# Optimization experiments

Hardware: AMD Instinct MI355X
Metric: run time of the kernel (lower is better)

The kernel has to match this reference:

```python
import jax, jax.numpy as jnp
import numpy as np

INPUT_DIM, HID, LAT, FUT = 32, 128, 64, 128
B, T = 1024, 512


def _linear(x, W, b):
    return x @ W.T + b


def _lstm_layer(xs, Wih, Whh, b):
    # xs: [T, B, D_in] -> ys: [T, B, HID], h_T: [B, HID]
    Bsz = xs.shape[1]
    h0 = jnp.zeros((Bsz, HID), xs.dtype)
    c0 = jnp.zeros((Bsz, HID), xs.dtype)

    def step(carry, xt):
        h, c = carry
        g = xt @ Wih.T + h @ Whh.T + b  # [B, 4*HID]
        i, f, gg, o = jnp.split(g, 4, axis=-1)  # torch gate order i,f,g,o
        i = jax.nn.sigmoid(i)
        f = jax.nn.sigmoid(f)
        gg = jnp.tanh(gg)
        o = jax.nn.sigmoid(o)
        c = f * c + i * gg
        h = o * jnp.tanh(c)
        return (h, c), h

    (hT, _), ys = jax.lax.scan(step, (h0, c0), xs)
    return ys, hT


def setup_inputs() -> dict:
    key = jax.random.key(0)
    ks = iter(jax.random.split(key, 40))

    def w(shape, scale=0.05):
        return (jax.random.normal(next(ks), shape, dtype=jnp.float32) * scale)

    inp = {
        "x": jax.random.normal(next(ks), (B, T, INPUT_DIM), dtype=jnp.float32),
        "eps": jax.random.normal(next(ks), (B, LAT), dtype=jnp.float32),
        "u": jax.random.uniform(next(ks), (B, LAT), dtype=jnp.float32, minval=1e-4, maxval=1 - 1e-4),
        "choice": jax.random.uniform(next(ks), (B,), dtype=jnp.float32),
        # 3-layer LSTM params (torch: W_ih [4H, D], W_hh [4H, H], fused bias)
        "Wih0": w((4 * HID, INPUT_DIM)), "Whh0": w((4 * HID, HID)), "b0": w((4 * HID,)),
        "Wih1": w((4 * HID, HID)), "Whh1": w((4 * HID, HID)), "b1": w((4 * HID,)),
        "Wih2": w((4 * HID, HID)), "Whh2": w((4 * HID, HID)), "b2": w((4 * HID,)),
        "ln_g": jnp.ones((HID,), jnp.float32), "ln_b": jnp.zeros((HID,), jnp.float32),
        "fc1_W": w((128, HID)), "fc1_b": w((128,)),
        "fc2_W": w((64, 128)), "fc2_b": w((64,)),
        "mean_W": w((LAT, 64)), "mean_b": w((LAT,)),
        "logvar_W": w((LAT, 64)), "logvar_b": w((LAT,)),
        "scale_W": w((LAT, 64)), "scale_b": w((LAT,)),
        "shape_W": w((LAT, 64)), "shape_b": w((LAT,)),
        "dec1_W": w((128, LAT)), "dec1_b": w((128,)),
        "dec2_W": w((500, 128)), "dec2_b": w((500,)),
        "out_W": w((FUT, 500)), "out_b": w((FUT,)),
        "pi_params": jnp.array([3.0, 0.01], jnp.float32),
    }
    return inp


def reference(x, eps, u, choice,
              Wih0, Whh0, b0, Wih1, Whh1, b1, Wih2, Whh2, b2,
              ln_g, ln_b, fc1_W, fc1_b, fc2_W, fc2_b,
              mean_W, mean_b, logvar_W, logvar_b,
              scale_W, scale_b, shape_W, shape_b,
              dec1_W, dec1_b, dec2_W, dec2_b, out_W, out_b, pi_params):
    # --- Encoder ---
    xs = jnp.transpose(x, (1, 0, 2))  # [T, B, D]
    ys, _ = _lstm_layer(xs, Wih0, Whh0, b0)
    ys, _ = _lstm_layer(ys, Wih1, Whh1, b1)
    _, h = _lstm_layer(ys, Wih2, Whh2, b2)  # final hidden of last layer [B, HID]
    mu = h.mean(-1, keepdims=True)
    var = jnp.mean((h - mu) ** 2, -1, keepdims=True)
    h = (h - mu) * jax.lax.rsqrt(var + 1e-5) * ln_g + ln_b
    hid = jax.nn.relu(_linear(h, fc1_W, fc1_b))
    hid = jax.nn.relu(_linear(hid, fc2_W, fc2_b))  # dropout = identity (eval)
    z_mean = _linear(hid, mean_W, mean_b)
    z_logvar = _linear(hid, logvar_W, logvar_b)
    z_scale = jnp.exp(_linear(hid, scale_W, scale_b))
    z_shape = jnp.maximum(_linear(hid, shape_W, shape_b), 1e-6)
    # --- Reparameterize (vectorized mixture select) ---
    z_gauss = z_mean + eps * jnp.exp(0.5 * z_logvar)
    z_gpd = z_scale / z_shape * ((1.0 - u) ** (-z_shape) - 1.0)
    pi = jax.nn.softmax(pi_params)
    z = jnp.where((choice < pi[0])[:, None], z_gauss, z_gpd)
    # --- Decoder ---
    d = jax.nn.relu(_linear(z, dec1_W, dec1_b))
    d = jax.nn.relu(_linear(d, dec2_W, dec2_b))  # dropout = identity (eval)
    rec = _linear(d, out_W, out_b)
    return rec, z_mean, z_logvar, z_scale, z_shape
```

## Files before the change

### kernel.cpp

```cpp
#include <hip/hip_runtime.h>
#include <math.h>

typedef __attribute__((ext_vector_type(8))) short s16x8;
typedef __attribute__((ext_vector_type(4))) float f32x4;
typedef unsigned long long ull;

constexpr float LOG2E = 1.4426950408889634f;

__device__ __forceinline__ unsigned short f2bf(float f) {
  unsigned int x = __builtin_bit_cast(unsigned int, f);
  x += 0x7fffu + ((x >> 16) & 1u);
  return (unsigned short)(x >> 16);
}
__device__ __forceinline__ float fexp2(float x) { return __builtin_amdgcn_exp2f(x); }
__device__ __forceinline__ float frcp(float x)  { return __builtin_amdgcn_rcpf(x); }

#define MFMA16(A, B, Cc) __builtin_amdgcn_mfma_f32_16x16x32_bf16((A), (B), (Cc), 0, 0, 0)

constexpr int TT = 512;
constexpr int NB = 1024;
constexpr int CH  = 2;
constexpr int PUB = 4;

template <int DIN, bool FIRST, bool LAST>
__device__ __forceinline__ void scan_layer(
    unsigned short* x_s,
    unsigned short* h_s,
    float* b_s,
    const float* __restrict__ xin,
    unsigned short* ys,
    const float* __restrict__ Wih, const float* __restrict__ Whh,
    const float* __restrict__ bias, float* __restrict__ hT,
    int* prog_in, int* prog_out, int bblk)
{
  constexpr int KTX = DIN / 32;
  constexpr int XM  = (DIN == 32) ? 3 : 7;
  const int tid = threadIdx.x;
  const int wv = tid >> 6, ln = tid & 63, l15 = ln & 15, lg = ln >> 4;
  const int row0 = bblk * 16;
  const int prow = tid >> 5, pcol = tid & 31;

  s16x8 bfx[4][KTX], bfh[4][4];
#pragma unroll
  for (int j = 0; j < 4; ++j) {
    const float sc = (j == 2) ? (2.0f * LOG2E) : (-LOG2E);
    const int n = j * 128 + wv * 16 + l15;
#pragma unroll
    for (int kt = 0; kt < KTX; ++kt) {
      s16x8 f;
#pragma unroll
      for (int e = 0; e < 8; ++e) f[e] = (short)f2bf(Wih[n * DIN + kt * 32 + lg * 8 + e] * sc);
      bfx[j][kt] = f;
    }
#pragma unroll
    for (int kt = 0; kt < 4; ++kt) {
      s16x8 f;
#pragma unroll
      for (int e = 0; e < 8; ++e) f[e] = (short)f2bf(Whh[n * 128 + kt * 32 + lg * 8 + e] * sc);
      bfh[j][kt] = f;
    }
  }
  b_s[tid] = bias[tid] * ((tid >> 7) == 2 ? 2.0f * LOG2E : -LOG2E);
  for (int i = tid; i < 2 * 16 * 128; i += 512) h_s[i] = 0;

  float xrf[CH];
  ull xrh[CH];
  int avail = 0;
  if (FIRST) {
#pragma unroll
    for (int s = 0; s < CH; ++s)
      xrf[s] = xin[(size_t)(row0 + prow) * (TT * 32) + s * 32 + pcol];
  } else {
    int ch;
    do { ch = __hip_atomic_load(prog_in, __ATOMIC_RELAXED, __HIP_MEMORY_SCOPE_AGENT); } while (ch * PUB < CH);
    avail = ch * PUB;
#pragma unroll
    for (int s = 0; s < CH; ++s)
      xrh[s] = __hip_atomic_load(
          (ull*)ys + ((size_t)s * (NB * 128) + (size_t)(row0 + prow) * 128 + pcol * 4) / 4,
          __ATOMIC_RELAXED, __HIP_MEMORY_SCOPE_AGENT);
  }
  __syncthreads();

  float cst[4] = {0.f, 0.f, 0.f, 0.f};
  const int hcol = wv * 16 + lg * 4;

  for (int t0 = 0; t0 < TT; t0 += CH) {
    if (FIRST) {
#pragma unroll
      for (int s = 0; s < CH; ++s)
        x_s[s * (16 * DIN) + prow * DIN + (pcol ^ ((prow & XM) << 3))] = f2bf(xrf[s]);
    } else {
#pragma unroll
      for (int s = 0; s < CH; ++s)
        *reinterpret_cast<ull*>(
            &x_s[s * (16 * DIN) + prow * DIN + ((pcol * 4) ^ ((prow & 7) << 3))]) = xrh[s];
    }
    __syncthreads();

    f32x4 gx[CH][4];
#pragma unroll
    for (int s = 0; s < CH; ++s) {
#pragma unroll
      for (int j = 0; j < 4; ++j)
        gx[s][j] = *reinterpret_cast<const f32x4*>(&b_s[j * 128 + wv * 16 + lg * 4]);
#pragma unroll
      for (int kt = 0; kt < KTX; ++kt) {
        const s16x8 xf = *reinterpret_cast<const s16x8*>(
            &x_s[s * (16 * DIN) + l15 * DIN + ((kt * 32 + lg * 8) ^ ((l15 & XM) << 3))]);
#pragma unroll
        for (int j = 0; j < 4; ++j) gx[s][j] = MFMA16(bfx[j][kt], xf, gx[s][j]);
      }
    }

    const int t1 = t0 + CH;
    if (t1 < TT) {
      if (FIRST) {
#pragma unroll
        for (int s = 0; s < CH; ++s)
          xrf[s] = xin[(size_t)(row0 + prow) * (TT * 32) + (t1 + s) * 32 + pcol];
      } else {
        if (avail < t1 + CH) {
          int ch;
          do { ch = __hip_atomic_load(prog_in, __ATOMIC_RELAXED, __HIP_MEMORY_SCOPE_AGENT); } while (ch * PUB < t1 + CH);
          avail = ch * PUB;
        }
#pragma unroll
        for (int s = 0; s < CH; ++s)
          xrh[s] = __hip_atomic_load(
              (ull*)ys + ((size_t)(t1 + s) * (NB * 128) + (size_t)(row0 + prow) * 128 + pcol * 4) / 4,
              __ATOMIC_RELAXED, __HIP_MEMORY_SCOPE_AGENT);
      }
    }

#pragma unroll
    for (int s = 0; s < CH; ++s) {
      const int t = t0 + s;
      if (s) __syncthreads();
      unsigned short* buf  = h_s + (t & 1) * (16 * 128);
      unsigned short* nbuf = h_s + ((t + 1) & 1) * (16 * 128);
      s16x8 afr[4];
#pragma unroll
      for (int kt = 0; kt < 4; ++kt)
        afr[kt] = *reinterpret_cast<const s16x8*>(
            &buf[l15 * 128 + ((kt * 32 + lg * 8) ^ ((l15 & 7) << 3))]);
      f32x4 acc[4];
#pragma unroll
      for (int j = 0; j < 4; ++j) acc[j] = gx[s][j];
#pragma unroll
      for (int kt = 0; kt < 4; ++kt)
#pragma unroll
        for (int j = 0; j < 4; ++j) acc[j] = MFMA16(bfh[j][kt], afr[kt], acc[j]);

      float hv[4];
#pragma unroll
      for (int r = 0; r < 4; ++r) {
        const float iv = frcp(1.0f + fexp2(acc[0][r]));
        const float fv = frcp(1.0f + fexp2(acc[1][r]));
        const float gv = 1.0f - 2.0f * frcp(1.0f + fexp2(acc[2][r]));
        const float ov = frcp(1.0f + fexp2(acc[3][r]));
        const float cn = fv * cst[r] + iv * gv;
        cst[r] = cn;
        const float th = 1.0f - 2.0f * frcp(1.0f + fexp2(cn * (2.0f * LOG2E)));
        hv[r] = ov * th;
      }
      unsigned int plo, phi;
      asm("v_cvt_pk_bf16_f32 %0, %1, %2" : "=v"(plo) : "v"(hv[0]), "v"(hv[1]));
      asm("v_cvt_pk_bf16_f32 %0, %1, %2" : "=v"(phi) : "v"(hv[2]), "v"(hv[3]));
      const ull hpack = (ull)plo | ((ull)phi << 32);

      *reinterpret_cast<ull*>(&nbuf[l15 * 128 + (hcol ^ ((l15 & 7) << 3))]) = hpack;

      if (!LAST) {
        __hip_atomic_store(
            (ull*)ys + ((size_t)t * (NB * 128) + (size_t)(row0 + l15) * 128 + hcol) / 4,
            hpack, __ATOMIC_RELAXED, __HIP_MEMORY_SCOPE_AGENT);
      } else if (t == TT - 1) {
        f32x4 o = {hv[0], hv[1], hv[2], hv[3]};
        *reinterpret_cast<f32x4*>(&hT[(row0 + l15) * 128 + hcol]) = o;
      }
    }

    if (!LAST && ((t0 + CH) % PUB) == 0) {
      asm volatile("s_waitcnt vmcnt(0)" ::: "memory");
      __syncthreads();
      if (tid == 0)
        __hip_atomic_store(prog_out, (t0 + CH) / PUB, __ATOMIC_RELAXED, __HIP_MEMORY_SCOPE_AGENT);
    } else {
      __syncthreads();
    }
  }
}

__global__ __launch_bounds__(512, 2) void lstm_fused(
    const float* __restrict__ x, unsigned short* ys,
    const float* __restrict__ Wih0, const float* __restrict__ Whh0, const float* __restrict__ b0,
    const float* __restrict__ Wih1, const float* __restrict__ Whh1, const float* __restrict__ b1,
    const float* __restrict__ Wih2, const float* __restrict__ Whh2, const float* __restrict__ b2,
    float* __restrict__ hT, int* prog)
{
  __shared__ unsigned short x_s[CH * 16 * 128];
  __shared__ unsigned short h_s[2 * 16 * 128];
  __shared__ float b_s[512];
  const int lay = blockIdx.x >> 6;
  const int bblk = blockIdx.x & 63;
  if (lay == 0) {
    scan_layer<32, true, false>(x_s, h_s, b_s, x, ys, Wih0, Whh0, b0, nullptr,
                                nullptr, &prog[(0 * 64 + bblk) * 16], bblk);
  } else if (lay == 1) {
    scan_layer<128, false, false>(x_s, h_s, b_s, nullptr, ys, Wih1, Whh1, b1, nullptr,
                                  &prog[(0 * 64 + bblk) * 16], &prog[(1 * 64 + bblk) * 16], bblk);
  } else {
    scan_layer<128, false, true>(x_s, h_s, b_s, nullptr, ys, Wih2, Whh2, b2, hT,
                                 &prog[(1 * 64 + bblk) * 16], nullptr, bblk);
  }
}

__global__ void init_flags(int* prog) {
  prog[threadIdx.x] = 0;
  prog[threadIdx.x + 1024] = 0;
}

__global__ __launch_bounds__(256) void head_kernel(
    const float* __restrict__ hT, const float* __restrict__ eps,
    const float* __restrict__ u, const float* __restrict__ choice,
    const float* __restrict__ ln_g, const float* __restrict__ ln_b,
    const float* __restrict__ fc1_W, const float* __restrict__ fc1_b,
    const float* __restrict__ fc2_W, const float* __restrict__ fc2_b,
    const float* __restrict__ mean_W, const float* __restrict__ mean_b,
    const float* __restrict__ logvar_W, const float* __restrict__ logvar_b,
    const float* __restrict__ scale_W, const float* __restrict__ scale_b,
    const float* __restrict__ shape_W, const float* __restrict__ shape_b,
    const float* __restrict__ dec1_W, const float* __restrict__ dec1_b,
    const float* __restrict__ dec2_W, const float* __restrict__ dec2_b,
    const float* __restrict__ out_W, const float* __restrict__ out_b,
    const float* __restrict__ pi_params, float* __restrict__ out)
{
  __shared__ float s_hn[4][128];
  __shared__ float s_a[4][128];
  __shared__ float s_b2[4][64];
  __shared__ float s_z[4][64];
  __shared__ float s_d1[4][128];
  __shared__ float s_d2[4][512];

  const int tid = threadIdx.x;
  const int gr0 = blockIdx.x * 4;

  {
    const int wvr = tid >> 6, lnn = tid & 63;
    const float v0 = hT[(gr0 + wvr) * 128 + lnn];
    const float v1 = hT[(gr0 + wvr) * 128 + 64 + lnn];
    float s = v0 + v1, s2 = v0 * v0 + v1 * v1;
#pragma unroll
    for (int off = 32; off; off >>= 1) {
      s  += __shfl_xor(s, off, 64);
      s2 += __shfl_xor(s2, off, 64);
    }
    const float mu  = s * (1.f / 128.f);
    const float var = s2 * (1.f / 128.f) - mu * mu;
    const float rs  = rsqrtf(var + 1e-5f);
    s_hn[wvr][lnn]      = (v0 - mu) * rs * ln_g[lnn]      + ln_b[lnn];
    s_hn[wvr][lnn + 64] = (v1 - mu) * rs * ln_g[lnn + 64] + ln_b[lnn + 64];
  }
  __syncthreads();
#pragma unroll
  for (int p = 0; p < 2; ++p) {
    const int idx = tid + p * 256, row = idx >> 7, col = idx & 127;
    const float* w = fc1_W + col * 128;
    float a = fc1_b[col];
    for (int k = 0; k < 128; k += 4)
      a += s_hn[row][k] * w[k] + s_hn[row][k + 1] * w[k + 1] +
           s_hn[row][k + 2] * w[k + 2] + s_hn[row][k + 3] * w[k + 3];
    s_a[row][col] = fmaxf(a, 0.f);
  }
  __syncthreads();
  {
    const int row = tid >> 6, col = tid & 63;
    const float* w = fc2_W + col * 128;
    float a = fc2_b[col];
    for (int k = 0; k < 128; ++k) a += s_a[row][k] * w[k];
    s_b2[row][col] = fmaxf(a, 0.f);
  }
  __syncthreads();
  {
    const int row = tid >> 6, c = tid & 63;
    const int gr = gr0 + row;
    float am = mean_b[c], al = logvar_b[c], as_ = scale_b[c], ah = shape_b[c];
    for (int k = 0; k < 64; ++k) {
      const float hv = s_b2[row][k];
      am  += hv * mean_W[c * 64 + k];
      al  += hv * logvar_W[c * 64 + k];
      as_ += hv * scale_W[c * 64 + k];
      ah  += hv * shape_W[c * 64 + k];
    }
    const float zsc = fexp2(as_ * LOG2E);
    const float zsh = fmaxf(ah, 1e-6f);
    out[131072 + gr * 64 + c] = am;
    out[196608 + gr * 64 + c] = al;
    out[262144 + gr * 64 + c] = zsc;
    out[327680 + gr * 64 + c] = zsh;
    const float ev = eps[gr * 64 + c], uv = u[gr * 64 + c], cv = choice[gr];
    const float zg = am + ev * fexp2(0.72134752044448170f * al);
    const float p0 = pi_params[0], p1 = pi_params[1];
    const float pi0 = 1.f / (1.f + expf(p1 - p0));
    const float tq = -zsh * logf(1.f - uv);
    const float zp = zsc * frcp(zsh) * expm1f(tq);
    s_z[row][c] = (cv < pi0) ? zg : zp;
  }
  __syncthreads();
#pragma unroll
  for (int p = 0; p < 2; ++p) {
    const int idx = tid + p * 256, row = idx >> 7, col = idx & 127;
    const float* w = dec1_W + col * 64;
    float a = dec1_b[col];
    for (int k = 0; k < 64; ++k) a += s_z[row][k] * w[k];
    s_d1[row][col] = fmaxf(a, 0.f);
  }
  __syncthreads();
  for (int o = tid; o < 2000; o += 256) {
    const int row = o / 500, col = o % 500;
    const float* w = dec2_W + col * 128;
    float a = dec2_b[col];
    for (int k = 0; k < 128; ++k) a += s_d1[row][k] * w[k];
    s_d2[row][col] = fmaxf(a, 0.f);
  }
  __syncthreads();
#pragma unroll
  for (int p = 0; p < 2; ++p) {
    const int idx = tid + p * 256, row = idx >> 7, col = idx & 127;
    const float* w = out_W + col * 500;
    float a = out_b[col];
    for (int k = 0; k < 500; ++k) a += s_d2[row][k] * w[k];
    out[(gr0 + row) * 128 + col] = a;
  }
}

extern "C" void kernel_launch(void* const* d_in, const int* in_sizes, int n_in,
                              void* d_out, int out_size, void* d_ws, size_t ws_size,
                              hipStream_t stream) {
  const float* x      = (const float*)d_in[0];
  const float* eps    = (const float*)d_in[1];
  const float* u      = (const float*)d_in[2];
  const float* choice = (const float*)d_in[3];
  const float* Wih0 = (const float*)d_in[4],  *Whh0 = (const float*)d_in[5],  *b0 = (const float*)d_in[6];
  const float* Wih1 = (const float*)d_in[7],  *Whh1 = (const float*)d_in[8],  *b1 = (const float*)d_in[9];
  const float* Wih2 = (const float*)d_in[10], *Whh2 = (const float*)d_in[11], *b2 = (const float*)d_in[12];
  const float* ln_g = (const float*)d_in[13], *ln_b = (const float*)d_in[14];
  const float* fc1_W = (const float*)d_in[15], *fc1_b = (const float*)d_in[16];
  const float* fc2_W = (const float*)d_in[17], *fc2_b = (const float*)d_in[18];
  const float* mean_W = (const float*)d_in[19], *mean_b = (const float*)d_in[20];
  const float* logvar_W = (const float*)d_in[21], *logvar_b = (const float*)d_in[22];
  const float* scale_W = (const float*)d_in[23], *scale_b = (const float*)d_in[24];
  const float* shape_W = (const float*)d_in[25], *shape_b = (const float*)d_in[26];
  const float* dec1_W = (const float*)d_in[27], *dec1_b = (const float*)d_in[28];
  const float* dec2_W = (const float*)d_in[29], *dec2_b = (const float*)d_in[30];
  const float* out_W = (const float*)d_in[31], *out_b = (const float*)d_in[32];
  const float* pi_params = (const float*)d_in[33];

  unsigned short* ys = (unsigned short*)d_ws;
  float* hT  = (float*)((char*)d_ws + (size_t)512 * 1024 * 128 * 2);
  int*   prog = (int*)((char*)d_ws + (size_t)512 * 1024 * 128 * 2 + (size_t)1024 * 128 * 4);

  init_flags<<<1, 1024, 0, stream>>>(prog);
  lstm_fused<<<192, 512, 0, stream>>>(x, ys, Wih0, Whh0, b0, Wih1, Whh1, b1,
                                      Wih2, Whh2, b2, hT, prog);
  head_kernel<<<256, 256, 0, stream>>>(hT, eps, u, choice, ln_g, ln_b,
      fc1_W, fc1_b, fc2_W, fc2_b, mean_W, mean_b, logvar_W, logvar_b,
      scale_W, scale_b, shape_W, shape_b, dec1_W, dec1_b, dec2_W, dec2_b,
      out_W, out_b, pi_params, (float*)d_out);
}
```

Baseline: 676.9 us.

## Restructure LSTM layer pipeline sync with lagged progress flags and fewer barriers

```diff
diff --git a/kernel.cpp b/kernel.cpp
--- a/kernel.cpp
+++ b/kernel.cpp
@@ -19,8 +19,14 @@
 
 constexpr int TT = 512;
 constexpr int NB = 1024;
-constexpr int CH  = 2;
-constexpr int PUB = 4;
+constexpr int CH = 2;
+
+__device__ __forceinline__ void bar_lgkm() {
+  __builtin_amdgcn_sched_barrier(0);
+  asm volatile("s_waitcnt lgkmcnt(0)" ::: "memory");
+  __builtin_amdgcn_s_barrier();
+  __builtin_amdgcn_sched_barrier(0);
+}
 
 template <int DIN, bool FIRST, bool LAST>
 __device__ __forceinline__ void scan_layer(
@@ -70,33 +76,34 @@
 #pragma unroll
     for (int s = 0; s < CH; ++s)
       xrf[s] = xin[(size_t)(row0 + prow) * (TT * 32) + s * 32 + pcol];
+#pragma unroll
+    for (int s = 0; s < CH; ++s)
+      x_s[s * (16 * DIN) + prow * DIN + (pcol ^ ((prow & XM) << 3))] = f2bf(xrf[s]);
   } else {
-    int ch;
-    do { ch = __hip_atomic_load(prog_in, __ATOMIC_RELAXED, __HIP_MEMORY_SCOPE_AGENT); } while (ch * PUB < CH);
-    avail = ch * PUB;
+    int f;
+    do { f = __hip_atomic_load(prog_in, __ATOMIC_RELAXED, __HIP_MEMORY_SCOPE_AGENT); } while (f < 1);
+    avail = f * CH;
 #pragma unroll
     for (int s = 0; s < CH; ++s)
       xrh[s] = __hip_atomic_load(
           (ull*)ys + ((size_t)s * (NB * 128) + (size_t)(row0 + prow) * 128 + pcol * 4) / 4,
           __ATOMIC_RELAXED, __HIP_MEMORY_SCOPE_AGENT);
-  }
-  __syncthreads();
+#pragma unroll
+    for (int s = 0; s < CH; ++s)
+      *reinterpret_cast<ull*>(
+          &x_s[s * (16 * DIN) + prow * DIN + ((pcol * 4) ^ ((prow & 7) << 3))]) = xrh[s];
+  }
+  bar_lgkm();
 
   float cst[4] = {0.f, 0.f, 0.f, 0.f};
   const int hcol = wv * 16 + lg * 4;
 
   for (int t0 = 0; t0 < TT; t0 += CH) {
-    if (FIRST) {
-#pragma unroll
-      for (int s = 0; s < CH; ++s)
-        x_s[s * (16 * DIN) + prow * DIN + (pcol ^ ((prow & XM) << 3))] = f2bf(xrf[s]);
-    } else {
-#pragma unroll
-      for (int s = 0; s < CH; ++s)
-        *reinterpret_cast<ull*>(
-            &x_s[s * (16 * DIN) + prow * DIN + ((pcol * 4) ^ ((prow & 7) << 3))]) = xrh[s];
-    }
-    __syncthreads();
+    const int t1 = t0 + CH;
+
+    int flag_early = 0;
+    if (!FIRST && t1 < TT)
+      flag_early = __hip_atomic_load(prog_in, __ATOMIC_RELAXED, __HIP_MEMORY_SCOPE_AGENT);
 
     f32x4 gx[CH][4];
 #pragma unroll
@@ -113,7 +120,6 @@
       }
     }
 
-    const int t1 = t0 + CH;
     if (t1 < TT) {
       if (FIRST) {
 #pragma unroll
@@ -121,9 +127,10 @@
           xrf[s] = xin[(size_t)(row0 + prow) * (TT * 32) + (t1 + s) * 32 + pcol];
       } else {
         if (avail < t1 + CH) {
-          int ch;
-          do { ch = __hip_atomic_load(prog_in, __ATOMIC_RELAXED, __HIP_MEMORY_SCOPE_AGENT); } while (ch * PUB < t1 + CH);
-          avail = ch * PUB;
+          int f = flag_early;
+          while (f * CH < t1 + CH)
+            f = __hip_atomic_load(prog_in, __ATOMIC_RELAXED, __HIP_MEMORY_SCOPE_AGENT);
+          avail = f * CH;
         }
 #pragma unroll
         for (int s = 0; s < CH; ++s)
@@ -136,7 +143,7 @@
 #pragma unroll
     for (int s = 0; s < CH; ++s) {
       const int t = t0 + s;
-      if (s) __syncthreads();
+      if (s) bar_lgkm();
       unsigned short* buf  = h_s + (t & 1) * (16 * 128);
       unsigned short* nbuf = h_s + ((t + 1) & 1) * (16 * 128);
       s16x8 afr[4];
@@ -181,14 +188,37 @@
       }
     }
 
-    if (!LAST && ((t0 + CH) % PUB) == 0) {
-      asm volatile("s_waitcnt vmcnt(0)" ::: "memory");
-      __syncthreads();
-      if (tid == 0)
-        __hip_atomic_store(prog_out, (t0 + CH) / PUB, __ATOMIC_RELAXED, __HIP_MEMORY_SCOPE_AGENT);
+    if (t1 < TT) {
+      if (FIRST) {
+#pragma unroll
+        for (int s = 0; s < CH; ++s)
+          x_s[s * (16 * DIN) + prow * DIN + (pcol ^ ((prow & XM) << 3))] = f2bf(xrf[s]);
+      } else {
+#pragma unroll
+        for (int s = 0; s < CH; ++s)
+          *reinterpret_cast<ull*>(
+              &x_s[s * (16 * DIN) + prow * DIN + ((pcol * 4) ^ ((prow & 7) << 3))]) = xrh[s];
+      }
+    }
+
+    if (!LAST) {
+      __builtin_amdgcn_sched_barrier(0);
+      if constexpr (FIRST) asm volatile("s_waitcnt vmcnt(4) lgkmcnt(0)" ::: "memory");
+      else                 asm volatile("s_waitcnt vmcnt(5) lgkmcnt(0)" ::: "memory");
+      __builtin_amdgcn_s_barrier();
+      __builtin_amdgcn_sched_barrier(0);
+      if (tid == 0 && t0 > 0)
+        __hip_atomic_store(prog_out, t0 / CH, __ATOMIC_RELAXED, __HIP_MEMORY_SCOPE_AGENT);
     } else {
-      __syncthreads();
-    }
+      bar_lgkm();
+    }
+  }
+
+  if (!LAST) {
+    asm volatile("s_waitcnt vmcnt(0)" ::: "memory");
+    __builtin_amdgcn_s_barrier();
+    if (tid == 0)
+      __hip_atomic_store(prog_out, TT / CH, __ATOMIC_RELAXED, __HIP_MEMORY_SCOPE_AGENT);
   }
 }
 
```

Result: slower. 730.9 us (+8.0%).

## Publish layer progress every chunk and restructure x staging to drop a barrier

Applied to the files above, without the earlier changes.

```diff
diff --git a/kernel.cpp b/kernel.cpp
--- a/kernel.cpp
+++ b/kernel.cpp
@@ -19,8 +19,7 @@
 
 constexpr int TT = 512;
 constexpr int NB = 1024;
-constexpr int CH  = 2;
-constexpr int PUB = 4;
+constexpr int CH = 2;
 
 template <int DIN, bool FIRST, bool LAST>
 __device__ __forceinline__ void scan_layer(
@@ -68,17 +67,22 @@
   int avail = 0;
   if (FIRST) {
 #pragma unroll
-    for (int s = 0; s < CH; ++s)
+    for (int s = 0; s < CH; ++s) {
       xrf[s] = xin[(size_t)(row0 + prow) * (TT * 32) + s * 32 + pcol];
+      x_s[s * (16 * DIN) + prow * DIN + (pcol ^ ((prow & XM) << 3))] = f2bf(xrf[s]);
+    }
   } else {
-    int ch;
-    do { ch = __hip_atomic_load(prog_in, __ATOMIC_RELAXED, __HIP_MEMORY_SCOPE_AGENT); } while (ch * PUB < CH);
-    avail = ch * PUB;
-#pragma unroll
-    for (int s = 0; s < CH; ++s)
+    int f;
+    do { f = __hip_atomic_load(prog_in, __ATOMIC_RELAXED, __HIP_MEMORY_SCOPE_AGENT); } while (f < 1);
+    avail = f * CH;
+#pragma unroll
+    for (int s = 0; s < CH; ++s) {
       xrh[s] = __hip_atomic_load(
           (ull*)ys + ((size_t)s * (NB * 128) + (size_t)(row0 + prow) * 128 + pcol * 4) / 4,
           __ATOMIC_RELAXED, __HIP_MEMORY_SCOPE_AGENT);
+      *reinterpret_cast<ull*>(
+          &x_s[s * (16 * DIN) + prow * DIN + ((pcol * 4) ^ ((prow & 7) << 3))]) = xrh[s];
+    }
   }
   __syncthreads();
 
@@ -86,51 +90,58 @@
   const int hcol = wv * 16 + lg * 4;
 
   for (int t0 = 0; t0 < TT; t0 += CH) {
-    if (FIRST) {
-#pragma unroll
-      for (int s = 0; s < CH; ++s)
-        x_s[s * (16 * DIN) + prow * DIN + (pcol ^ ((prow & XM) << 3))] = f2bf(xrf[s]);
-    } else {
-#pragma unroll
-      for (int s = 0; s < CH; ++s)
-        *reinterpret_cast<ull*>(
-            &x_s[s * (16 * DIN) + prow * DIN + ((pcol * 4) ^ ((prow & 7) << 3))]) = xrh[s];
-    }
-    __syncthreads();
-
-    f32x4 gx[CH][4];
-#pragma unroll
-    for (int s = 0; s < CH; ++s) {
-#pragma unroll
-      for (int j = 0; j < 4; ++j)
-        gx[s][j] = *reinterpret_cast<const f32x4*>(&b_s[j * 128 + wv * 16 + lg * 4]);
-#pragma unroll
-      for (int kt = 0; kt < KTX; ++kt) {
-        const s16x8 xf = *reinterpret_cast<const s16x8*>(
-            &x_s[s * (16 * DIN) + l15 * DIN + ((kt * 32 + lg * 8) ^ ((l15 & XM) << 3))]);
-#pragma unroll
-        for (int j = 0; j < 4; ++j) gx[s][j] = MFMA16(bfx[j][kt], xf, gx[s][j]);
-      }
-    }
-
     const int t1 = t0 + CH;
+
+    if (!LAST && tid == 0 && t0 > 0)
+      __hip_atomic_store(prog_out, t0 / CH, __ATOMIC_RELAXED, __HIP_MEMORY_SCOPE_AGENT);
+
+    int f_new = 0;
+    if (!FIRST && t1 < TT)
+      f_new = __hip_atomic_load(prog_in, __ATOMIC_RELAXED, __HIP_MEMORY_SCOPE_AGENT);
+
+    bool prefetched = false;
     if (t1 < TT) {
       if (FIRST) {
 #pragma unroll
         for (int s = 0; s < CH; ++s)
           xrf[s] = xin[(size_t)(row0 + prow) * (TT * 32) + (t1 + s) * 32 + pcol];
-      } else {
-        if (avail < t1 + CH) {
-          int ch;
-          do { ch = __hip_atomic_load(prog_in, __ATOMIC_RELAXED, __HIP_MEMORY_SCOPE_AGENT); } while (ch * PUB < t1 + CH);
-          avail = ch * PUB;
-        }
+        prefetched = true;
+      } else if (avail >= t1 + CH) {
 #pragma unroll
         for (int s = 0; s < CH; ++s)
           xrh[s] = __hip_atomic_load(
               (ull*)ys + ((size_t)(t1 + s) * (NB * 128) + (size_t)(row0 + prow) * 128 + pcol * 4) / 4,
               __ATOMIC_RELAXED, __HIP_MEMORY_SCOPE_AGENT);
-      }
+        prefetched = true;
+      }
+    }
+
+    f32x4 gx[CH][4];
+#pragma unroll
+    for (int s = 0; s < CH; ++s) {
+#pragma unroll
+      for (int j = 0; j < 4; ++j)
+        gx[s][j] = *reinterpret_cast<const f32x4*>(&b_s[j * 128 + wv * 16 + lg * 4]);
+#pragma unroll
+      for (int kt = 0; kt < KTX; ++kt) {
+        const s16x8 xf = *reinterpret_cast<const s16x8*>(
+            &x_s[s * (16 * DIN) + l15 * DIN + ((kt * 32 + lg * 8) ^ ((l15 & XM) << 3))]);
+#pragma unroll
+        for (int j = 0; j < 4; ++j) gx[s][j] = MFMA16(bfx[j][kt], xf, gx[s][j]);
+      }
+    }
+
+    if (t1 < TT && !prefetched) {
+      int f = f_new;
+      while (f * CH < t1 + CH)
+        f = __hip_atomic_load(prog_in, __ATOMIC_RELAXED, __HIP_MEMORY_SCOPE_AGENT);
+      f_new = f;
+      avail = f * CH;
+#pragma unroll
+      for (int s = 0; s < CH; ++s)
+        xrh[s] = __hip_atomic_load(
+            (ull*)ys + ((size_t)(t1 + s) * (NB * 128) + (size_t)(row0 + prow) * 128 + pcol * 4) / 4,
+            __ATOMIC_RELAXED, __HIP_MEMORY_SCOPE_AGENT);
     }
 
 #pragma unroll
@@ -179,17 +190,31 @@
         f32x4 o = {hv[0], hv[1], hv[2], hv[3]};
         *reinterpret_cast<f32x4*>(&hT[(row0 + l15) * 128 + hcol]) = o;
       }
-    }
-
-    if (!LAST && ((t0 + CH) % PUB) == 0) {
-      asm volatile("s_waitcnt vmcnt(0)" ::: "memory");
-      __syncthreads();
-      if (tid == 0)
-        __hip_atomic_store(prog_out, (t0 + CH) / PUB, __ATOMIC_RELAXED, __HIP_MEMORY_SCOPE_AGENT);
-    } else {
-      __syncthreads();
-    }
-  }
+
+      if (s == CH - 1 && t1 < TT) {
+        if (FIRST) {
+#pragma unroll
+          for (int ss = 0; ss < CH; ++ss)
+            x_s[ss * (16 * DIN) + prow * DIN + (pcol ^ ((prow & XM) << 3))] = f2bf(xrf[ss]);
+        } else {
+#pragma unroll
+          for (int ss = 0; ss < CH; ++ss)
+            *reinterpret_cast<ull*>(
+                &x_s[ss * (16 * DIN) + prow * DIN + ((pcol * 4) ^ ((prow & 7) << 3))]) = xrh[ss];
+        }
+      }
+    }
+
+    if (!FIRST && t1 < TT) {
+      const int a2 = f_new * CH;
+      if (a2 > avail) avail = a2;
+    }
+
+    __syncthreads();
+  }
+
+  if (!LAST && tid == 0)
+    __hip_atomic_store(prog_out, TT / CH, __ATOMIC_RELAXED, __HIP_MEMORY_SCOPE_AGENT);
 }
 
 __global__ __launch_bounds__(512, 2) void lstm_fused(
```

New measurement: 655.2 us. 3.2% less time.

## Publish LSTM layer progress every step with delayed stores and double-buffered inputs

Applied to the files above, without the earlier changes.

```diff
diff --git a/kernel.cpp b/kernel.cpp
--- a/kernel.cpp
+++ b/kernel.cpp
@@ -19,8 +19,6 @@
 
 constexpr int TT = 512;
 constexpr int NB = 1024;
-constexpr int CH  = 2;
-constexpr int PUB = 4;
 
 template <int DIN, bool FIRST, bool LAST>
 __device__ __forceinline__ void scan_layer(
@@ -38,157 +36,162 @@
   const int tid = threadIdx.x;
   const int wv = tid >> 6, ln = tid & 63, l15 = ln & 15, lg = ln >> 4;
   const int row0 = bblk * 16;
-  const int prow = tid >> 5, pcol = tid & 31;
+  const int sr = tid >> 5, sc = tid & 31;
 
   s16x8 bfx[4][KTX], bfh[4][4];
 #pragma unroll
   for (int j = 0; j < 4; ++j) {
-    const float sc = (j == 2) ? (2.0f * LOG2E) : (-LOG2E);
+    const float scale = (j == 2) ? (2.0f * LOG2E) : (-LOG2E);
     const int n = j * 128 + wv * 16 + l15;
 #pragma unroll
     for (int kt = 0; kt < KTX; ++kt) {
       s16x8 f;
 #pragma unroll
-      for (int e = 0; e < 8; ++e) f[e] = (short)f2bf(Wih[n * DIN + kt * 32 + lg * 8 + e] * sc);
+      for (int e = 0; e < 8; ++e) f[e] = (short)f2bf(Wih[n * DIN + kt * 32 + lg * 8 + e] * scale);
       bfx[j][kt] = f;
     }
 #pragma unroll
     for (int kt = 0; kt < 4; ++kt) {
       s16x8 f;
 #pragma unroll
-      for (int e = 0; e < 8; ++e) f[e] = (short)f2bf(Whh[n * 128 + kt * 32 + lg * 8 + e] * sc);
+      for (int e = 0; e < 8; ++e) f[e] = (short)f2bf(Whh[n * 128 + kt * 32 + lg * 8 + e] * scale);
       bfh[j][kt] = f;
     }
   }
   b_s[tid] = bias[tid] * ((tid >> 7) == 2 ? 2.0f * LOG2E : -LOG2E);
   for (int i = tid; i < 2 * 16 * 128; i += 512) h_s[i] = 0;
 
-  float xrf[CH];
-  ull xrh[CH];
+  float xrf = 0.f;
+  ull xrh = 0ull;
   int avail = 0;
   if (FIRST) {
-#pragma unroll
-    for (int s = 0; s < CH; ++s)
-      xrf[s] = xin[(size_t)(row0 + prow) * (TT * 32) + s * 32 + pcol];
+    xrf = xin[(size_t)(row0 + sr) * (TT * 32) + sc];
+    x_s[sr * DIN + (sc ^ ((sr & XM) << 3))] = f2bf(xrf);
   } else {
-    int ch;
-    do { ch = __hip_atomic_load(prog_in, __ATOMIC_RELAXED, __HIP_MEMORY_SCOPE_AGENT); } while (ch * PUB < CH);
-    avail = ch * PUB;
-#pragma unroll
-    for (int s = 0; s < CH; ++s)
-      xrh[s] = __hip_atomic_load(
-          (ull*)ys + ((size_t)s * (NB * 128) + (size_t)(row0 + prow) * 128 + pcol * 4) / 4,
-          __ATOMIC_RELAXED, __HIP_MEMORY_SCOPE_AGENT);
+    int f;
+    do { f = __hip_atomic_load(prog_in, __ATOMIC_RELAXED, __HIP_MEMORY_SCOPE_AGENT); } while (f < 1);
+    avail = f;
+    xrh = __hip_atomic_load(
+        (ull*)ys + ((size_t)(row0 + sr) * 128 + sc * 4) / 4,
+        __ATOMIC_RELAXED, __HIP_MEMORY_SCOPE_AGENT);
+    *reinterpret_cast<ull*>(&x_s[sr * DIN + ((sc * 4) ^ ((sr & 7) << 3))]) = xrh;
   }
   __syncthreads();
 
   float cst[4] = {0.f, 0.f, 0.f, 0.f};
   const int hcol = wv * 16 + lg * 4;
-
-  for (int t0 = 0; t0 < TT; t0 += CH) {
-    if (FIRST) {
-#pragma unroll
-      for (int s = 0; s < CH; ++s)
-        x_s[s * (16 * DIN) + prow * DIN + (pcol ^ ((prow & XM) << 3))] = f2bf(xrf[s]);
-    } else {
-#pragma unroll
-      for (int s = 0; s < CH; ++s)
+  ull held = 0ull;
+
+  for (int t = 0; t < TT; ++t) {
+    if (!LAST) {
+      if (tid == 0 && t >= 2)
+        __hip_atomic_store(prog_out, t - 1, __ATOMIC_RELAXED, __HIP_MEMORY_SCOPE_AGENT);
+      if (t > 0)
+        __hip_atomic_store(
+            (ull*)ys + ((size_t)(t - 1) * (NB * 128) + (size_t)(row0 + l15) * 128 + hcol) / 4,
+            held, __ATOMIC_RELAXED, __HIP_MEMORY_SCOPE_AGENT);
+    }
+
+    int f_new = 0;
+    if (!FIRST && t + 1 < TT)
+      f_new = __hip_atomic_load(prog_in, __ATOMIC_RELAXED, __HIP_MEMORY_SCOPE_AGENT);
+
+    bool pf = false;
+    if (t + 1 < TT) {
+      if (FIRST) {
+        xrf = xin[(size_t)(row0 + sr) * (TT * 32) + (t + 1) * 32 + sc];
+        pf = true;
+      } else if (avail >= t + 2) {
+        xrh = __hip_atomic_load(
+            (ull*)ys + ((size_t)(t + 1) * (NB * 128) + (size_t)(row0 + sr) * 128 + sc * 4) / 4,
+            __ATOMIC_RELAXED, __HIP_MEMORY_SCOPE_AGENT);
+        pf = true;
+      }
+    }
+
+    const unsigned short* xbuf = x_s + (t & 1) * (16 * DIN);
+    f32x4 gx[4];
+#pragma unroll
+    for (int j = 0; j < 4; ++j)
+      gx[j] = *reinterpret_cast<const f32x4*>(&b_s[j * 128 + wv * 16 + lg * 4]);
+#pragma unroll
+    for (int kt = 0; kt < KTX; ++kt) {
+      const s16x8 xf = *reinterpret_cast<const s16x8*>(
+          &xbuf[l15 * DIN + ((kt * 32 + lg * 8) ^ ((l15 & XM) << 3))]);
+#pragma unroll
+      for (int j = 0; j < 4; ++j) gx[j] = MFMA16(bfx[j][kt], xf, gx[j]);
+    }
+
+    if (!FIRST && t + 1 < TT && !pf) {
+      int f = f_new;
+      while (f < t + 2)
+        f = __hip_atomic_load(prog_in, __ATOMIC_RELAXED, __HIP_MEMORY_SCOPE_AGENT);
+      f_new = f;
+      xrh = __hip_atomic_load(
+          (ull*)ys + ((size_t)(t + 1) * (NB * 128) + (size_t)(row0 + sr) * 128 + sc * 4) / 4,
+          __ATOMIC_RELAXED, __HIP_MEMORY_SCOPE_AGENT);
+    }
+
+    const unsigned short* hbuf = h_s + (t & 1) * (16 * 128);
+    unsigned short* nbuf = h_s + ((t + 1) & 1) * (16 * 128);
+    s16x8 afr[4];
+#pragma unroll
+    for (int kt = 0; kt < 4; ++kt)
+      afr[kt] = *reinterpret_cast<const s16x8*>(
+          &hbuf[l15 * 128 + ((kt * 32 + lg * 8) ^ ((l15 & 7) << 3))]);
+#pragma unroll
+    for (int kt = 0; kt < 4; ++kt)
+#pragma unroll
+      for (int j = 0; j < 4; ++j) gx[j] = MFMA16(bfh[j][kt], afr[kt], gx[j]);
+
+    float hv[4];
+#pragma unroll
+    for (int r = 0; r < 4; ++r) {
+      const float iv = frcp(1.0f + fexp2(gx[0][r]));
+      const float fv = frcp(1.0f + fexp2(gx[1][r]));
+      const float gv = 1.0f - 2.0f * frcp(1.0f + fexp2(gx[2][r]));
+      const float ov = frcp(1.0f + fexp2(gx[3][r]));
+      const float cn = fv * cst[r] + iv * gv;
+      cst[r] = cn;
+      const float th = 1.0f - 2.0f * frcp(1.0f + fexp2(cn * (2.0f * LOG2E)));
+      hv[r] = ov * th;
+    }
+    unsigned int plo, phi;
+    asm("v_cvt_pk_bf16_f32 %0, %1, %2" : "=v"(plo) : "v"(hv[0]), "v"(hv[1]));
+    asm("v_cvt_pk_bf16_f32 %0, %1, %2" : "=v"(phi) : "v"(hv[2]), "v"(hv[3]));
+    const ull hpack = (ull)plo | ((ull)phi << 32);
+
+    *reinterpret_cast<ull*>(&nbuf[l15 * 128 + (hcol ^ ((l15 & 7) << 3))]) = hpack;
+
+    if (!LAST) {
+      held = hpack;
+    } else if (t == TT - 1) {
+      f32x4 o = {hv[0], hv[1], hv[2], hv[3]};
+      *reinterpret_cast<f32x4*>(&hT[(row0 + l15) * 128 + hcol]) = o;
+    }
+
+    if (t + 1 < TT) {
+      if (FIRST) {
+        x_s[((t + 1) & 1) * (16 * DIN) + sr * DIN + (sc ^ ((sr & XM) << 3))] = f2bf(xrf);
+      } else {
         *reinterpret_cast<ull*>(
-            &x_s[s * (16 * DIN) + prow * DIN + ((pcol * 4) ^ ((prow & 7) << 3))]) = xrh[s];
-    }
+            &x_s[((t + 1) & 1) * (16 * DIN) + sr * DIN + ((sc * 4) ^ ((sr & 7) << 3))]) = xrh;
+      }
+    }
+
+    if (!FIRST && f_new > avail) avail = f_new;
+
     __syncthreads();
-
-    f32x4 gx[CH][4];
-#pragma unroll
-    for (int s = 0; s < CH; ++s) {
-#pragma unroll
-      for (int j = 0; j < 4; ++j)
-        gx[s][j] = *reinterpret_cast<const f32x4*>(&b_s[j * 128 + wv * 16 + lg * 4]);
-#pragma unroll
-      for (int kt = 0; kt < KTX; ++kt) {
-        const s16x8 xf = *reinterpret_cast<const s16x8*>(
-            &x_s[s * (16 * DIN) + l15 * DIN + ((kt * 32 + lg * 8) ^ ((l15 & XM) << 3))]);
-#pragma unroll
-        for (int j = 0; j < 4; ++j) gx[s][j] = MFMA16(bfx[j][kt], xf, gx[s][j]);
-      }
-    }
-
-    const int t1 = t0 + CH;
-    if (t1 < TT) {
-      if (FIRST) {
-#pragma unroll
-        for (int s = 0; s < CH; ++s)
-          xrf[s] = xin[(size_t)(row0 + prow) * (TT * 32) + (t1 + s) * 32 + pcol];
-      } else {
-        if (avail < t1 + CH) {
-          int ch;
-          do { ch = __hip_atomic_load(prog_in, __ATOMIC_RELAXED, __HIP_MEMORY_SCOPE_AGENT); } while (ch * PUB < t1 + CH);
-          avail = ch * PUB;
-        }
-#pragma unroll
-        for (int s = 0; s < CH; ++s)
-          xrh[s] = __hip_atomic_load(
-              (ull*)ys + ((size_t)(t1 + s) * (NB * 128) + (size_t)(row0 + prow) * 128 + pcol * 4) / 4,
-              __ATOMIC_RELAXED, __HIP_MEMORY_SCOPE_AGENT);
-      }
-    }
-
-#pragma unroll
-    for (int s = 0; s < CH; ++s) {
-      const int t = t0 + s;
-      if (s) __syncthreads();
-      unsigned short* buf  = h_s + (t & 1) * (16 * 128);
-      unsigned short* nbuf = h_s + ((t + 1) & 1) * (16 * 128);
-      s16x8 afr[4];
-#pragma unroll
-      for (int kt = 0; kt < 4; ++kt)
-        afr[kt] = *reinterpret_cast<const s16x8*>(
-            &buf[l15 * 128 + ((kt * 32 + lg * 8) ^ ((l15 & 7) << 3))]);
-      f32x4 acc[4];
-#pragma unroll
-      for (int j = 0; j < 4; ++j) acc[j] = gx[s][j];
-#pragma unroll
-      for (int kt = 0; kt < 4; ++kt)
-#pragma unroll
-        for (int j = 0; j < 4; ++j) acc[j] = MFMA16(bfh[j][kt], afr[kt], acc[j]);
-
-      float hv[4];
-#pragma unroll
-      for (int r = 0; r < 4; ++r) {
-        const float iv = frcp(1.0f + fexp2(acc[0][r]));
-        const float fv = frcp(1.0f + fexp2(acc[1][r]));
-        const float gv = 1.0f - 2.0f * frcp(1.0f + fexp2(acc[2][r]));
-        const float ov = frcp(1.0f + fexp2(acc[3][r]));
-        const float cn = fv * cst[r] + iv * gv;
-        cst[r] = cn;
-        const float th = 1.0f - 2.0f * frcp(1.0f + fexp2(cn * (2.0f * LOG2E)));
-        hv[r] = ov * th;
-      }
-      unsigned int plo, phi;
-      asm("v_cvt_pk_bf16_f32 %0, %1, %2" : "=v"(plo) : "v"(hv[0]), "v"(hv[1]));
-      asm("v_cvt_pk_bf16_f32 %0, %1, %2" : "=v"(phi) : "v"(hv[2]), "v"(hv[3]));
-      const ull hpack = (ull)plo | ((ull)phi << 32);
-
-      *reinterpret_cast<ull*>(&nbuf[l15 * 128 + (hcol ^ ((l15 & 7) << 3))]) = hpack;
-
-      if (!LAST) {
-        __hip_atomic_store(
-            (ull*)ys + ((size_t)t * (NB * 128) + (size_t)(row0 + l15) * 128 + hcol) / 4,
-            hpack, __ATOMIC_RELAXED, __HIP_MEMORY_SCOPE_AGENT);
-      } else if (t == TT - 1) {
-        f32x4 o = {hv[0], hv[1], hv[2], hv[3]};
-        *reinterpret_cast<f32x4*>(&hT[(row0 + l15) * 128 + hcol]) = o;
-      }
-    }
-
-    if (!LAST && ((t0 + CH) % PUB) == 0) {
-      asm volatile("s_waitcnt vmcnt(0)" ::: "memory");
-      __syncthreads();
-      if (tid == 0)
-        __hip_atomic_store(prog_out, (t0 + CH) / PUB, __ATOMIC_RELAXED, __HIP_MEMORY_SCOPE_AGENT);
-    } else {
-      __syncthreads();
-    }
+  }
+
+  if (!LAST) {
+    __hip_atomic_store(
+        (ull*)ys + ((size_t)(TT - 1) * (NB * 128) + (size_t)(row0 + l15) * 128 + hcol) / 4,
+        held, __ATOMIC_RELAXED, __HIP_MEMORY_SCOPE_AGENT);
+    asm volatile("s_waitcnt vmcnt(0)" ::: "memory");
+    __syncthreads();
+    if (tid == 0)
+      __hip_atomic_store(prog_out, TT, __ATOMIC_RELAXED, __HIP_MEMORY_SCOPE_AGENT);
   }
 }
 
@@ -199,7 +202,7 @@
     const float* __restrict__ Wih2, const float* __restrict__ Whh2, const float* __restrict__ b2,
     float* __restrict__ hT, int* prog)
 {
-  __shared__ unsigned short x_s[CH * 16 * 128];
+  __shared__ unsigned short x_s[2 * 16 * 128];
   __shared__ unsigned short h_s[2 * 16 * 128];
   __shared__ float b_s[512];
   const int lay = blockIdx.x >> 6;
```

Result: slower. 939.3 us (+38.8%).
